# Performance work log

Measured on AMD Instinct MI355X. Metric: run time of the kernel, lower is better.

## Reference

```python
import jax, jax.numpy as jnp
import numpy as np

TOP_K = 10  # hardcoded k in the original tf.math.top_k call
EPS = 1e-8


def _make_boxes(key, n):
    # valid xyxy boxes in a ~1024x1024 image
    k1, k2 = jax.random.split(key)
    xy = jax.random.uniform(k1, (n, 2), dtype=jnp.float32) * 900.0
    wh = jax.random.uniform(k2, (n, 2), dtype=jnp.float32) * 120.0 + 4.0
    return jnp.concatenate([xy, xy + wh], axis=-1)


def _pairwise_iou(a, b):
    # a: [N,4] xyxy, b: [M,4] xyxy -> [N,M]
    lt = jnp.maximum(a[:, None, :2], b[None, :, :2])  # [N,M,2]
    rb = jnp.minimum(a[:, None, 2:], b[None, :, 2:])  # [N,M,2]
    wh = jnp.clip(rb - lt, 0.0)
    inter = wh[..., 0] * wh[..., 1]                    # [N,M]
    area_a = (a[:, 2] - a[:, 0]) * (a[:, 3] - a[:, 1])  # [N]
    area_b = (b[:, 2] - b[:, 0]) * (b[:, 3] - b[:, 1])  # [M]
    union = area_a[:, None] + area_b[None, :] - inter
    return inter / (union + EPS)


def setup_inputs() -> dict:
    key = jax.random.key(0)
    k1, k2, k3, k4 = jax.random.split(key, 4)
    N, M, C = 16384, 2048, 81
    proposals = _make_boxes(k1, N)
    gt_proposals = _make_boxes(k2, M)
    cls_prob = jax.random.uniform(k3, (N, C), dtype=jnp.float32)
    gt_cls = jax.random.randint(k4, (M,), 0, C, dtype=jnp.int32)
    return {"proposals": proposals, "cls_prob": cls_prob,
            "gt_proposals": gt_proposals, "gt_cls": gt_cls}


def reference(proposals, cls_prob, gt_proposals, gt_cls):
    # Reachable math of ProposalTargetLayer.call (the original aborts via
    # embed()/exit() right after building the top-k mask `i`).
    iou = _pairwise_iou(proposals, gt_proposals)          # [N,M]
    flat = jnp.reshape(iou, (-1,))
    _, top_idx = jax.lax.top_k(flat, TOP_K)
    # tensor_scatter_nd_update of ones onto a zero tensor -> boolean top-k mask
    mask_flat = jnp.zeros_like(flat).at[top_idx].set(1.0)
    mask = jnp.reshape(mask_flat, iou.shape).astype(jnp.bool_)  # [N,M]
    return (iou, mask)
```

## Files before the change

kernel.cpp:

```cpp
#include <hip/hip_runtime.h>

#define TOPK 10
#define BLK 256
#define ROWS_PER_BLOCK 8
#define CAND_CAP 32768
#define SLACK 1e-5f

__device__ __forceinline__ bool better(float v1, int i1, float v2, int i2) {
    return (v1 > v2) || (v1 == v2 && i1 < i2);
}

__device__ __forceinline__ void insert10(float (&lv)[TOPK], int (&li)[TOPK],
                                         float v, int ix, float& mv, int& mi) {
    int ws = 0; float wv = lv[0]; int wi = li[0];
#pragma unroll
    for (int j = 1; j < TOPK; ++j)
        if (better(wv, wi, lv[j], li[j])) { wv = lv[j]; wi = li[j]; ws = j; }
#pragma unroll
    for (int j = 0; j < TOPK; ++j)
        if (j == ws) { lv[j] = v; li[j] = ix; }
    mv = lv[0]; mi = li[0];
#pragma unroll
    for (int j = 1; j < TOPK; ++j)
        if (better(mv, mi, lv[j], li[j])) { mv = lv[j]; mi = li[j]; }
}

__device__ __forceinline__ void waveReduceTop10(float (&lv)[TOPK], int (&li)[TOPK],
                                                float* wcv, int* wci, int tid) {
    const int wave = tid >> 6;
    const int lane = tid & 63;
    for (int r = 0; r < TOPK; ++r) {
        float bv = lv[0]; int bi = li[0];
#pragma unroll
        for (int j = 1; j < TOPK; ++j)
            if (better(lv[j], li[j], bv, bi)) { bv = lv[j]; bi = li[j]; }
#pragma unroll
        for (int off = 32; off >= 1; off >>= 1) {
            float ov = __shfl_xor(bv, off, 64);
            int   oi = __shfl_xor(bi, off, 64);
            if (better(ov, oi, bv, bi)) { bv = ov; bi = oi; }
        }
#pragma unroll
        for (int j = 0; j < TOPK; ++j)
            if (lv[j] == bv && li[j] == bi) { lv[j] = -2.0f; li[j] = 0x7fffffff; }
        if (lane == 0) { wcv[wave * TOPK + r] = bv; wci[wave * TOPK + r] = bi; }
    }
}

template <typename EmitFn>
__device__ __forceinline__ void wave0FinalTop10(const float* wcv, const int* wci,
                                                int tid, EmitFn emit) {
    float v = (tid < 40) ? wcv[tid] : -2.0f;
    int   ix = (tid < 40) ? wci[tid] : 0x7fffffff;
    for (int r = 0; r < TOPK; ++r) {
        float bv = v; int bi = ix;
#pragma unroll
        for (int off = 32; off >= 1; off >>= 1) {
            float ov = __shfl_xor(bv, off, 64);
            int   oi = __shfl_xor(bi, off, 64);
            if (better(ov, oi, bv, bi)) { bv = ov; bi = oi; }
        }
        if (v == bv && ix == bi) { v = -2.0f; ix = 0x7fffffff; }
        if (tid == 0) emit(r, bv, bi);
    }
}

__device__ __forceinline__ float iou_exact(const float4 a, const float aA,
                                           const float4 b, const float bA) {
    const float ltx = fmaxf(a.x, b.x);
    const float lty = fmaxf(a.y, b.y);
    const float rbx = fminf(a.z, b.z);
    const float rby = fminf(a.w, b.w);
    const float w = fmaxf(rbx - ltx, 0.0f);
    const float h = fmaxf(rby - lty, 0.0f);
    const float inter = __fmul_rn(w, h);
    const float s = aA + bA;
    const float uni = s - inter;
    const float den = uni + 1e-8f;
    return inter / den;
}

__device__ __forceinline__ float iou_approx(const float4 a, const float aA,
                                            const float4 b, const float bA) {
    const float ltx = fmaxf(a.x, b.x);
    const float lty = fmaxf(a.y, b.y);
    const float rbx = fminf(a.z, b.z);
    const float rby = fminf(a.w, b.w);
    const float w = fmaxf(rbx - ltx, 0.0f);
    const float h = fmaxf(rby - lty, 0.0f);
    const float inter = __fmul_rn(w, h);
    const float den = (aA + bA - inter) + 1e-8f;
    return inter * __builtin_amdgcn_rcpf(den);
}

__global__ __launch_bounds__(BLK) void blockmax_kernel(
    const float4* __restrict__ prop, const float4* __restrict__ gt,
    float* __restrict__ blockmax, int N, int M) {
    const int tid = threadIdx.x;
    const int bid = blockIdx.x;
    const int row0 = bid * ROWS_PER_BLOCK;
    const int M4 = M & ~3;
    float vmax = -2.0f;

    for (int m0 = 4 * tid; m0 < M4; m0 += 4 * BLK) {
        const float4 b0 = gt[m0 + 0], b1 = gt[m0 + 1], b2 = gt[m0 + 2], b3 = gt[m0 + 3];
        const float bA0 = __fmul_rn(b0.z - b0.x, b0.w - b0.y);
        const float bA1 = __fmul_rn(b1.z - b1.x, b1.w - b1.y);
        const float bA2 = __fmul_rn(b2.z - b2.x, b2.w - b2.y);
        const float bA3 = __fmul_rn(b3.z - b3.x, b3.w - b3.y);
#pragma unroll
        for (int nl = 0; nl < ROWS_PER_BLOCK; ++nl) {
            const int row = row0 + nl;
            if (row < N) {
                const float4 a = prop[row];
                const float aA = __fmul_rn(a.z - a.x, a.w - a.y);
                vmax = fmaxf(vmax, iou_approx(a, aA, b0, bA0));
                vmax = fmaxf(vmax, iou_approx(a, aA, b1, bA1));
                vmax = fmaxf(vmax, iou_approx(a, aA, b2, bA2));
                vmax = fmaxf(vmax, iou_approx(a, aA, b3, bA3));
            }
        }
    }
    for (int m = M4 + tid; m < M; m += BLK) {
        const float4 b = gt[m];
        const float bA = __fmul_rn(b.z - b.x, b.w - b.y);
#pragma unroll
        for (int nl = 0; nl < ROWS_PER_BLOCK; ++nl) {
            const int row = row0 + nl;
            if (row < N) {
                const float4 a = prop[row];
                const float aA = __fmul_rn(a.z - a.x, a.w - a.y);
                vmax = fmaxf(vmax, iou_approx(a, aA, b, bA));
            }
        }
    }

    __shared__ float sred[4];
#pragma unroll
    for (int off = 32; off >= 1; off >>= 1)
        vmax = fmaxf(vmax, __shfl_xor(vmax, off, 64));
    if ((tid & 63) == 0) sred[tid >> 6] = vmax;
    __syncthreads();
    if (tid == 0)
        blockmax[bid] = fmaxf(fmaxf(sred[0], sred[1]), fmaxf(sred[2], sred[3]));
}

__global__ __launch_bounds__(BLK) void threshold_kernel(
    const float* __restrict__ blockmax, int nb,
    float* __restrict__ tm_ptr, int* __restrict__ cand_cnt) {
    __shared__ float wcv[4 * TOPK];
    __shared__ int   wci[4 * TOPK];
    const int tid = threadIdx.x;

    float lv[TOPK]; int li[TOPK];
#pragma unroll
    for (int j = 0; j < TOPK; ++j) { lv[j] = -2.0f; li[j] = 0x7fffffff; }
    float mv = -2.0f; int mi = 0x7fffffff;

    for (int i = tid; i < nb; i += BLK) {
        const float v = blockmax[i];
        if (better(v, i, mv, mi)) insert10(lv, li, v, i, mv, mi);
    }
    waveReduceTop10(lv, li, wcv, wci, tid);
    __syncthreads();
    if (tid < 64) {
        wave0FinalTop10(wcv, wci, tid, [&](int r, float bv, int bi) {
            (void)bi;
            if (r == TOPK - 1) *tm_ptr = bv - SLACK;
        });
    }
    if (tid == 0) *cand_cnt = 0;
}

__global__ __launch_bounds__(BLK) void iou_main_kernel(
    const float4* __restrict__ prop, const float4* __restrict__ gt,
    float* __restrict__ iou_out, float* __restrict__ mask_out,
    const float* __restrict__ tm_ptr, int* __restrict__ cand_cnt,
    int* __restrict__ cand_idx, int N, int M) {
    const int tid = threadIdx.x;
    const int bid = blockIdx.x;
    const int row0 = bid * ROWS_PER_BLOCK;
    const float Tm = *tm_ptr;
    const int M4 = M & ~3;
    const float4 zero4 = make_float4(0.0f, 0.0f, 0.0f, 0.0f);

    for (int m0 = 4 * tid; m0 < M4; m0 += 4 * BLK) {
        const float4 b0 = gt[m0 + 0], b1 = gt[m0 + 1], b2 = gt[m0 + 2], b3 = gt[m0 + 3];
        const float bA0 = __fmul_rn(b0.z - b0.x, b0.w - b0.y);
        const float bA1 = __fmul_rn(b1.z - b1.x, b1.w - b1.y);
        const float bA2 = __fmul_rn(b2.z - b2.x, b2.w - b2.y);
        const float bA3 = __fmul_rn(b3.z - b3.x, b3.w - b3.y);
#pragma unroll
        for (int nl = 0; nl < ROWS_PER_BLOCK; ++nl) {
            const int row = row0 + nl;
            if (row < N) {
                const float4 a = prop[row];
                const float aA = __fmul_rn(a.z - a.x, a.w - a.y);
                const float i0 = iou_exact(a, aA, b0, bA0);
                const float i1 = iou_exact(a, aA, b1, bA1);
                const float i2 = iou_exact(a, aA, b2, bA2);
                const float i3 = iou_exact(a, aA, b3, bA3);
                const long long base = (long long)row * M + m0;
                *reinterpret_cast<float4*>(iou_out + base) = make_float4(i0, i1, i2, i3);
                *reinterpret_cast<float4*>(mask_out + base) = zero4;
                if (i0 >= Tm || i1 >= Tm || i2 >= Tm || i3 >= Tm) {
                    if (i0 >= Tm) { int s = atomicAdd(cand_cnt, 1); if (s < CAND_CAP) cand_idx[s] = (int)base; }
                    if (i1 >= Tm) { int s = atomicAdd(cand_cnt, 1); if (s < CAND_CAP) cand_idx[s] = (int)base + 1; }
                    if (i2 >= Tm) { int s = atomicAdd(cand_cnt, 1); if (s < CAND_CAP) cand_idx[s] = (int)base + 2; }
                    if (i3 >= Tm) { int s = atomicAdd(cand_cnt, 1); if (s < CAND_CAP) cand_idx[s] = (int)base + 3; }
                }
            }
        }
    }
    for (int m = M4 + tid; m < M; m += BLK) {
        const float4 b = gt[m];
        const float bA = __fmul_rn(b.z - b.x, b.w - b.y);
#pragma unroll
        for (int nl = 0; nl < ROWS_PER_BLOCK; ++nl) {
            const int row = row0 + nl;
            if (row < N) {
                const float4 a = prop[row];
                const float aA = __fmul_rn(a.z - a.x, a.w - a.y);
                const float v = iou_exact(a, aA, b, bA);
                const long long idx = (long long)row * M + m;
                iou_out[idx] = v;
                mask_out[idx] = 0.0f;
                if (v >= Tm) { int s = atomicAdd(cand_cnt, 1); if (s < CAND_CAP) cand_idx[s] = (int)idx; }
            }
        }
    }
}

__global__ __launch_bounds__(BLK) void final_kernel(
    const int* __restrict__ cand_cnt, const int* __restrict__ cand_idx,
    const float* __restrict__ iou_out, float* __restrict__ mask_out) {
    __shared__ float wcv[4 * TOPK];
    __shared__ int   wci[4 * TOPK];
    const int tid = threadIdx.x;
    int c = *cand_cnt;
    if (c > CAND_CAP) c = CAND_CAP;

    float lv[TOPK]; int li[TOPK];
#pragma unroll
    for (int j = 0; j < TOPK; ++j) { lv[j] = -2.0f; li[j] = 0x7fffffff; }
    float mv = -2.0f; int mi = 0x7fffffff;

    for (int i = tid; i < c; i += BLK) {
        const int idx = cand_idx[i];
        const float v = iou_out[idx];
        if (better(v, idx, mv, mi)) insert10(lv, li, v, idx, mv, mi);
    }
    waveReduceTop10(lv, li, wcv, wci, tid);
    __syncthreads();
    if (tid < 64) {
        wave0FinalTop10(wcv, wci, tid, [&](int r, float bv, int bi) {
            (void)r;
            if (bi >= 0 && bi != 0x7fffffff && bv >= 0.0f) mask_out[bi] = 1.0f;
        });
    }
}

extern "C" void kernel_launch(void* const* d_in, const int* in_sizes, int n_in,
                              void* d_out, int out_size, void* d_ws, size_t ws_size,
                              hipStream_t stream) {
    const float4* prop = (const float4*)d_in[0];
    const float4* gt = (const float4*)d_in[2];
    const int N = in_sizes[0] / 4;
    const int M = in_sizes[2] / 4;

    float* iou_out = (float*)d_out;
    float* mask_out = iou_out + (long long)N * M;

    const int nblocks = (N + ROWS_PER_BLOCK - 1) / ROWS_PER_BLOCK;

    char* ws = (char*)d_ws;
    float* blockmax = (float*)ws;
    float* tm_ptr = (float*)(ws + 16384);
    int* cand_cnt = (int*)(ws + 16388);
    int* cand_idx = (int*)(ws + 16392);

    blockmax_kernel<<<nblocks, BLK, 0, stream>>>(prop, gt, blockmax, N, M);
    threshold_kernel<<<1, BLK, 0, stream>>>(blockmax, nblocks, tm_ptr, cand_cnt);
    iou_main_kernel<<<nblocks, BLK, 0, stream>>>(prop, gt, iou_out, mask_out,
                                                 tm_ptr, cand_cnt, cand_idx, N, M);
    final_kernel<<<1, BLK, 0, stream>>>(cand_cnt, cand_idx, iou_out, mask_out);
}
```

Measured before the change: 94.34 us.

## Replace exhaustive per-block IoU max with sparse sampled max for threshold

The first pass previously computed the exact max IoU over all M columns for each 8-row block, so the threshold kernel could derive a top-k cutoff. Now each block evaluates only 256 sampled (row, column) pairs and takes their max as a lower bound. The threshold built from these samples is still a valid lower bound for the top-10 candidate filtering, but it is looser. That loosening may produce many more candidates in the main kernel, and could overflow CAND_CAP. The goal is to drop a full extra N×M IoU pass.

Result: faster. 86.91 us (-7.9%).

```diff
diff --git a/kernel.cpp b/kernel.cpp
--- a/kernel.cpp
+++ b/kernel.cpp
@@ -93,53 +93,29 @@
     return inter * __builtin_amdgcn_rcpf(den);
 }
 
-__global__ __launch_bounds__(BLK) void blockmax_kernel(
+__global__ __launch_bounds__(BLK) void sample_max_kernel(
     const float4* __restrict__ prop, const float4* __restrict__ gt,
     float* __restrict__ blockmax, int N, int M) {
     const int tid = threadIdx.x;
     const int bid = blockIdx.x;
-    const int row0 = bid * ROWS_PER_BLOCK;
-    const int M4 = M & ~3;
-    float vmax = -2.0f;
-
-    for (int m0 = 4 * tid; m0 < M4; m0 += 4 * BLK) {
-        const float4 b0 = gt[m0 + 0], b1 = gt[m0 + 1], b2 = gt[m0 + 2], b3 = gt[m0 + 3];
-        const float bA0 = __fmul_rn(b0.z - b0.x, b0.w - b0.y);
-        const float bA1 = __fmul_rn(b1.z - b1.x, b1.w - b1.y);
-        const float bA2 = __fmul_rn(b2.z - b2.x, b2.w - b2.y);
-        const float bA3 = __fmul_rn(b3.z - b3.x, b3.w - b3.y);
-#pragma unroll
-        for (int nl = 0; nl < ROWS_PER_BLOCK; ++nl) {
-            const int row = row0 + nl;
-            if (row < N) {
-                const float4 a = prop[row];
-                const float aA = __fmul_rn(a.z - a.x, a.w - a.y);
-                vmax = fmaxf(vmax, iou_approx(a, aA, b0, bA0));
-                vmax = fmaxf(vmax, iou_approx(a, aA, b1, bA1));
-                vmax = fmaxf(vmax, iou_approx(a, aA, b2, bA2));
-                vmax = fmaxf(vmax, iou_approx(a, aA, b3, bA3));
-            }
-        }
-    }
-    for (int m = M4 + tid; m < M; m += BLK) {
-        const float4 b = gt[m];
+    const int row = bid * ROWS_PER_BLOCK + (tid & 7);
+    long long c = ((long long)(tid >> 3) * M) >> 5;
+    const int col = (int)((c + (bid & 63)) % M);
+
+    float v = -2.0f;
+    if (row < N) {
+        const float4 a = prop[row];
+        const float aA = __fmul_rn(a.z - a.x, a.w - a.y);
+        const float4 b = gt[col];
         const float bA = __fmul_rn(b.z - b.x, b.w - b.y);
-#pragma unroll
-        for (int nl = 0; nl < ROWS_PER_BLOCK; ++nl) {
-            const int row = row0 + nl;
-            if (row < N) {
-                const float4 a = prop[row];
-                const float aA = __fmul_rn(a.z - a.x, a.w - a.y);
-                vmax = fmaxf(vmax, iou_approx(a, aA, b, bA));
-            }
-        }
+        v = iou_approx(a, aA, b, bA);
     }
 
     __shared__ float sred[4];
 #pragma unroll
     for (int off = 32; off >= 1; off >>= 1)
-        vmax = fmaxf(vmax, __shfl_xor(vmax, off, 64));
-    if ((tid & 63) == 0) sred[tid >> 6] = vmax;
+        v = fmaxf(v, __shfl_xor(v, off, 64));
+    if ((tid & 63) == 0) sred[tid >> 6] = v;
     __syncthreads();
     if (tid == 0)
         blockmax[bid] = fmaxf(fmaxf(sred[0], sred[1]), fmaxf(sred[2], sred[3]));
@@ -279,7 +255,7 @@
     int* cand_cnt = (int*)(ws + 16388);
     int* cand_idx = (int*)(ws + 16392);
 
-    blockmax_kernel<<<nblocks, BLK, 0, stream>>>(prop, gt, blockmax, N, M);
+    sample_max_kernel<<<nblocks, BLK, 0, stream>>>(prop, gt, blockmax, N, M);
     threshold_kernel<<<1, BLK, 0, stream>>>(blockmax, nblocks, tm_ptr, cand_cnt);
     iou_main_kernel<<<nblocks, BLK, 0, stream>>>(prop, gt, iou_out, mask_out,
                                                  tm_ptr, cand_cnt, cand_idx, N, M);
```
